# Kernel optimization log

Measured on AMD Instinct MI355X. Metric: run time of the kernel, lower is better.

## Reference

```python
import jax, jax.numpy as jnp
import numpy as np

HIDDEN = 1024
HEADS = 16
HEAD_DIM = HIDDEN // HEADS  # 64
ROPE_BASE = 10000.0
CLAMP = 10000.0


def _rope_cos_sin(seq_len, dtype=jnp.float32):
    inv_freq = 1.0 / (ROPE_BASE ** (jnp.arange(0, HEAD_DIM, 2, dtype=dtype) / HEAD_DIM))
    t = jnp.arange(seq_len, dtype=dtype)
    freqs = jnp.outer(t, inv_freq)  # [T, HEAD_DIM//2]
    return jnp.cos(freqs), jnp.sin(freqs)


def _apply_rope(x, cos, sin):
    # x: [B, H, T, HEAD_DIM]; cos/sin: [T, HEAD_DIM//2]
    x1, x2 = jnp.split(x, 2, axis=-1)
    cos = cos[None, None]
    sin = sin[None, None]
    return jnp.concatenate([x1 * cos - x2 * sin, x1 * sin + x2 * cos], axis=-1)


def setup_inputs() -> dict:
    key = jax.random.key(0)
    ks = jax.random.split(key, 5)
    B, T, D = 2, 2048, HIDDEN
    x = jax.random.normal(ks[0], (B, T, D), dtype=jnp.float32)
    # torch Linear weights are [out, in]; init std=0.02, zero bias
    Wq = jax.random.normal(ks[1], (D, D), dtype=jnp.float32) * 0.02
    Wk = jax.random.normal(ks[2], (D, D), dtype=jnp.float32) * 0.02
    Wv = jax.random.normal(ks[3], (D, D), dtype=jnp.float32) * 0.02
    Wo = jax.random.normal(ks[4], (D, D), dtype=jnp.float32) * 0.02
    bq = jnp.zeros((D,), jnp.float32)
    bk = jnp.zeros((D,), jnp.float32)
    bv = jnp.zeros((D,), jnp.float32)
    bo = jnp.zeros((D,), jnp.float32)
    # causal mask: True where attention is disallowed (strict upper triangle)
    causal_mask = jnp.triu(jnp.ones((T, T), dtype=bool), k=1)[None, None]
    return {"x": x, "causal_mask": causal_mask,
            "Wq": Wq, "bq": bq, "Wk": Wk, "bk": bk,
            "Wv": Wv, "bv": bv, "Wo": Wo, "bo": bo}


def reference(x, causal_mask, Wq, bq, Wk, bk, Wv, bv, Wo, bo):
    B, T, D = x.shape
    H, hd = HEADS, HEAD_DIM

    def proj(W, b):
        y = jnp.einsum('btd,ed->bte', x, W) + b
        return y.reshape(B, T, H, hd).transpose(0, 2, 1, 3)  # [B,H,T,hd]

    q = proj(Wq, bq)
    k = proj(Wk, bk)
    v = proj(Wv, bv)

    cos, sin = _rope_cos_sin(T, x.dtype)
    q = _apply_rope(q, cos, sin)
    k = _apply_rope(k, cos, sin)

    scores = jnp.einsum('bhqd,bhkd->bhqk', q, k) / jnp.sqrt(jnp.asarray(hd, x.dtype))
    # masked_fill(-inf) happens BEFORE clamp, so masked entries become -10000
    scores = jnp.where(causal_mask[:, :, :T, :T], -jnp.inf, scores)
    scores = jnp.clip(scores, -CLAMP, CLAMP)
    attn = jax.nn.softmax(scores, axis=-1)
    out = jnp.einsum('bhqk,bhkd->bhqd', attn, v)
    out = out.transpose(0, 2, 1, 3).reshape(B, T, D)
    return jnp.einsum('btd,ed->bte', out, Wo) + bo
```

## Files before the change

kernel.cpp:

```cpp
#include <hip/hip_runtime.h>
#include <hip/hip_bf16.h>
#include <math.h>

#define T_SEQ   2048
#define D_MOD   1024
#define N_HEADS 16
#define HEAD_DIM 64
#define B_BATCH 2
#define M_ROWS  (B_BATCH * T_SEQ)

typedef unsigned short u16;
typedef unsigned int u32;
typedef __attribute__((ext_vector_type(8))) short short8;
typedef __attribute__((ext_vector_type(4))) float floatx4;
typedef __attribute__((ext_vector_type(16))) float f32x16;
typedef __attribute__((ext_vector_type(4))) u32 u32x4;

__device__ inline floatx4 mfma16(short8 a, short8 b, floatx4 c) {
  return __builtin_amdgcn_mfma_f32_16x16x32_bf16(a, b, c, 0, 0, 0);
}
__device__ inline f32x16 mfma32(short8 a, short8 b, f32x16 c) {
  return __builtin_amdgcn_mfma_f32_32x32x16_bf16(a, b, c, 0, 0, 0);
}

__device__ inline u16 f2bf(float f) {
  __hip_bfloat16 h = __float2bfloat16(f);
  return __builtin_bit_cast(u16, h);
}
__device__ inline u32 pack2bf(float lo, float hi) {
  return (u32)f2bf(lo) | ((u32)f2bf(hi) << 16);
}

__device__ inline void gload16(const void* g, void* s) {
  __builtin_amdgcn_global_load_lds(
      (const __attribute__((address_space(1))) void*)g,
      (__attribute__((address_space(3))) void*)s, 16, 0, 0);
}

__global__ void cast_all_kernel(const float* __restrict__ x,
                                const float* __restrict__ Wq, const float* __restrict__ Wk,
                                const float* __restrict__ Wv, const float* __restrict__ Wo,
                                u16* __restrict__ Xb, u16* __restrict__ Wqb, u16* __restrict__ Wkb,
                                u16* __restrict__ Wvb, u16* __restrict__ Wob) {
  size_t i4 = ((size_t)blockIdx.x * 256 + threadIdx.x) * 4;
  size_t seg = i4 >> 20;
  const float* src; u16* dst; size_t off;
  if (seg < 4)       { src = x;  dst = Xb;  off = i4; }
  else if (seg == 4) { src = Wq; dst = Wqb; off = i4 - ((size_t)4 << 20); }
  else if (seg == 5) { src = Wk; dst = Wkb; off = i4 - ((size_t)5 << 20); }
  else if (seg == 6) { src = Wv; dst = Wvb; off = i4 - ((size_t)6 << 20); }
  else               { src = Wo; dst = Wob; off = i4 - ((size_t)7 << 20); }
  float4 v = *(const float4*)(src + off);
  ushort4 o;
  o.x = f2bf(v.x); o.y = f2bf(v.y); o.z = f2bf(v.z); o.w = f2bf(v.w);
  *(ushort4*)(dst + off) = o;
}

__global__ void rope_table_kernel(float* __restrict__ cosT, float* __restrict__ sinT) {
  int tid = blockIdx.x * blockDim.x + threadIdx.x;
  int t = tid >> 5, j = tid & 31;
  double inv = pow(10000.0, -((double)(2 * j) / 64.0));
  double a = (double)t * inv;
  cosT[tid] = (float)cos(a);
  sinT[tid] = (float)sin(a);
}

template<int OUT_BF16, int DO_ROPE>
__global__ __launch_bounds__(256) void gemm128_kernel(
    const u16* __restrict__ A,
    const u16* __restrict__ W0, const u16* __restrict__ W1, const u16* __restrict__ W2,
    const float* __restrict__ b0, const float* __restrict__ b1, const float* __restrict__ b2,
    void* __restrict__ C0, void* __restrict__ C1, void* __restrict__ C2,
    const float* __restrict__ cosT, const float* __restrict__ sinT) {
  const int z = blockIdx.z;
  const u16*  W    = (z == 0) ? W0 : (z == 1 ? W1 : W2);
  const float* bias = (z == 0) ? b0 : (z == 1 ? b1 : b2);
  void*       C    = (z == 0) ? C0 : (z == 1 ? C1 : C2);
  const int K = D_MOD, N = D_MOD;

  __shared__ __align__(16) char smem[34816];
  u16* lA0 = (u16*)smem;
  u16* lA1 = (u16*)(smem + 8192);
  u16* lB0 = (u16*)(smem + 16384);
  u16* lB1 = (u16*)(smem + 24576);

  const int tid = threadIdx.x;
  const int w = tid >> 6, l = tid & 63, g = l >> 4, ln = l & 15;
  const int wr = w >> 1, wc = w & 1;
  const int m0 = blockIdx.y * 128, n0 = blockIdx.x * 128;

  floatx4 acc[4][4];
#pragma unroll
  for (int mi = 0; mi < 4; ++mi)
#pragma unroll
    for (int ni = 0; ni < 4; ++ni) acc[mi][ni] = (floatx4){0.f, 0.f, 0.f, 0.f};

  auto stage = [&](u16* la, u16* lb, int kk) {
#pragma unroll
    for (int p = 0; p < 2; ++p) {
      int c = p * 256 + w * 64 + l;
      int r = c >> 2, cc = c & 3;
      gload16(A + (size_t)(m0 + r) * K + kk + cc * 8, la + (p * 256 + w * 64) * 8);
      gload16(W + (size_t)(n0 + r) * K + kk + cc * 8, lb + (p * 256 + w * 64) * 8);
    }
  };

  stage(lA0, lB0, 0);
  __syncthreads();
  for (int t = 0; t < K / 32; ++t) {
    u16* la = (t & 1) ? lA1 : lA0;
    u16* lb = (t & 1) ? lB1 : lB0;
    if (t + 1 < K / 32) stage((t & 1) ? lA0 : lA1, (t & 1) ? lB0 : lB1, (t + 1) * 32);
    short8 af[4], bf[4];
#pragma unroll
    for (int mi = 0; mi < 4; ++mi)
      af[mi] = *(const short8*)&la[(wr * 64 + mi * 16 + ln) * 32 + g * 8];
#pragma unroll
    for (int ni = 0; ni < 4; ++ni)
      bf[ni] = *(const short8*)&lb[(wc * 64 + ni * 16 + ln) * 32 + g * 8];
#pragma unroll
    for (int mi = 0; mi < 4; ++mi)
#pragma unroll
      for (int ni = 0; ni < 4; ++ni)
        acc[mi][ni] = mfma16(af[mi], bf[ni], acc[mi][ni]);
    __syncthreads();
  }

  float bv[4];
#pragma unroll
  for (int ni = 0; ni < 4; ++ni) bv[ni] = bias[n0 + wc * 64 + ni * 16 + ln];

  if (DO_ROPE && z == 2) {
    u16* pt = (u16*)smem;
#pragma unroll
    for (int mi = 0; mi < 4; ++mi)
#pragma unroll
      for (int ni = 0; ni < 4; ++ni)
#pragma unroll
        for (int r = 0; r < 4; ++r)
          pt[(wc * 64 + ni * 16 + ln) * 136 + wr * 64 + mi * 16 + g * 4 + r] =
              f2bf(acc[mi][ni][r] + bv[ni]);
    __syncthreads();
    u16* Vt = (u16*)C;
    const int b = m0 >> 11, tc0 = m0 & (T_SEQ - 1);
#pragma unroll
    for (int i = 0; i < 8; ++i) {
      const int c = tid + 256 * i;
      const int row = c >> 4, mc = c & 15;
      const int n = n0 + row;
      const int hh = n >> 6, d = n & 63;
      short8 val = *(const short8*)&pt[row * 136 + mc * 8];
      *(short8*)(Vt + ((size_t)(b * N_HEADS + hh) * 64 + d) * T_SEQ + tc0 + mc * 8) = val;
    }
    return;
  }

#pragma unroll
  for (int mi = 0; mi < 4; ++mi) {
#pragma unroll
    for (int r = 0; r < 4; ++r) {
      const int m = m0 + wr * 64 + mi * 16 + g * 4 + r;
      if (DO_ROPE && z < 2) {
        const int t = m & (T_SEQ - 1);
#pragma unroll
        for (int ni = 0; ni < 2; ++ni) {
          const int j = ni * 16 + ln;
          float cv = cosT[t * 32 + j], sv = sinT[t * 32 + j];
          float v1 = acc[mi][ni][r] + bv[ni];
          float v2 = acc[mi][ni + 2][r] + bv[ni + 2];
          ((u16*)C)[(size_t)m * N + n0 + wc * 64 + j]      = f2bf(v1 * cv - v2 * sv);
          ((u16*)C)[(size_t)m * N + n0 + wc * 64 + j + 32] = f2bf(v1 * sv + v2 * cv);
        }
      } else {
#pragma unroll
        for (int ni = 0; ni < 4; ++ni) {
          float v = acc[mi][ni][r] + bv[ni];
          size_t idx = (size_t)m * N + n0 + wc * 64 + ni * 16 + ln;
          if (OUT_BF16) ((u16*)C)[idx] = f2bf(v);
          else          ((float*)C)[idx] = v;
        }
      }
    }
  }
}

__global__ __launch_bounds__(256) void flash7_kernel(const u16* __restrict__ Q, const u16* __restrict__ Kb,
                                                     const u16* __restrict__ Vt, u16* __restrict__ O) {
  __shared__ float og[3][32][64];
  __shared__ float mlg[3][2][64];

  const int tid = threadIdx.x;
  const int w = tid >> 6, l = tid & 63;
  const int lq = l & 31, hi = l >> 5;

  const int orig = blockIdx.x;
  const int wg = (orig & 7) * 256 + (orig >> 3);
  const int bh = wg >> 6;
  const int qt = 63 - (wg & 63);
  const int q0 = qt * 32;
  const int b = bh >> 4, h = bh & 15;

  const u16* Qh = Q  + (size_t)b * T_SEQ * D_MOD + h * HEAD_DIM;
  const u16* Kh = Kb + (size_t)b * T_SEQ * D_MOD + h * HEAD_DIM;
  const u16* Vh = Vt + (size_t)bh * 64 * T_SEQ;

  short8 qf[4];
  {
    const u16* qp = Qh + (size_t)(q0 + lq) * D_MOD + 8 * hi;
#pragma unroll
    for (int j = 0; j < 4; ++j) qf[j] = *(const short8*)(qp + 16 * j);
  }

  f32x16 o0, o1;
#pragma unroll
  for (int r = 0; r < 16; ++r) { o0[r] = 0.f; o1[r] = 0.f; }
  float m_r = -INFINITY, l_r = 0.f;

  const int ntiles = (qt >> 1) + 1;
  for (int kt = w; kt < ntiles; kt += 4) {
    const int k0 = kt * 64;
    const bool last = (kt == ntiles - 1);

    short8 kf0[4], kf1[4], vf0[4], vf1[4];
    {
      const u16* kp0 = Kh + (size_t)(k0 + lq) * D_MOD + 8 * hi;
      const u16* kp1 = kp0 + 32 * D_MOD;
#pragma unroll
      for (int j = 0; j < 4; ++j) {
        kf0[j] = *(const short8*)(kp0 + 16 * j);
        kf1[j] = *(const short8*)(kp1 + 16 * j);
      }
      const u16* vp0 = Vh + (size_t)lq * T_SEQ + k0 + 8 * hi;
      const u16* vp1 = vp0 + 32 * T_SEQ;
#pragma unroll
      for (int js = 0; js < 4; ++js) {
        vf0[js] = *(const short8*)(vp0 + 16 * js);
        vf1[js] = *(const short8*)(vp1 + 16 * js);
      }
    }

    f32x16 s0, s1;
#pragma unroll
    for (int r = 0; r < 16; ++r) { s0[r] = 0.f; s1[r] = 0.f; }
    __builtin_amdgcn_s_setprio(1);
#pragma unroll
    for (int j = 0; j < 4; ++j) {
      s0 = mfma32(kf0[j], qf[j], s0);
      s1 = mfma32(kf1[j], qf[j], s1);
    }
    __builtin_amdgcn_s_setprio(0);

    float p[32];
#pragma unroll
    for (int r = 0; r < 16; ++r) { p[r] = s0[r] * 0.125f; p[16 + r] = s1[r] * 0.125f; }
    if (last) {
      const int qrow = q0 + lq;
#pragma unroll
      for (int r = 0; r < 16; ++r) {
        const int kv = k0 + (r & 3) + 8 * (r >> 2) + 4 * hi;
        if (kv > qrow) p[r] = -10000.0f;
        if (kv + 32 > qrow) p[16 + r] = -10000.0f;
      }
    }

    float mx = p[0];
#pragma unroll
    for (int i = 1; i < 32; ++i) mx = fmaxf(mx, p[i]);
    mx = fmaxf(mx, __shfl_xor(mx, 32));

    const float mnew = fmaxf(m_r, mx);
    const float alpha = __expf(m_r - mnew);
    l_r *= alpha;
#pragma unroll
    for (int r = 0; r < 16; ++r) { o0[r] *= alpha; o1[r] *= alpha; }
    m_r = mnew;
#pragma unroll
    for (int i = 0; i < 32; ++i) p[i] = __expf(p[i] - m_r);
    float sum = 0.f;
#pragma unroll
    for (int i = 0; i < 32; ++i) sum += p[i];
    sum += __shfl_xor(sum, 32);
    l_r += sum;

    u32x4 fw[4];
#pragma unroll
    for (int a = 0; a < 2; ++a) {
      u32 W[8];
#pragma unroll
      for (int j = 0; j < 8; ++j) W[j] = pack2bf(p[16 * a + 2 * j], p[16 * a + 2 * j + 1]);
      u32 A0 = __shfl_xor(hi ? W[0] : W[2], 32);
      u32 A1 = __shfl_xor(hi ? W[1] : W[3], 32);
      u32 B0 = __shfl_xor(hi ? W[4] : W[6], 32);
      u32 B1 = __shfl_xor(hi ? W[5] : W[7], 32);
      fw[2 * a]     = (u32x4){hi ? A0 : W[0], hi ? A1 : W[1], hi ? W[2] : A0, hi ? W[3] : A1};
      fw[2 * a + 1] = (u32x4){hi ? B0 : W[4], hi ? B1 : W[5], hi ? W[6] : B0, hi ? W[7] : B1};
    }

    __builtin_amdgcn_s_setprio(1);
#pragma unroll
    for (int js = 0; js < 4; ++js) {
      short8 pf = __builtin_bit_cast(short8, fw[js]);
      o0 = mfma32(vf0[js], pf, o0);
      o1 = mfma32(vf1[js], pf, o1);
    }
    __builtin_amdgcn_s_setprio(0);
  }

  if (w > 0) {
    mlg[w - 1][0][l] = m_r;
    mlg[w - 1][1][l] = l_r;
#pragma unroll
    for (int r = 0; r < 16; ++r) {
      og[w - 1][r][l]      = o0[r];
      og[w - 1][16 + r][l] = o1[r];
    }
  }
  __syncthreads();
  if (w != 0) return;

  float m = m_r;
#pragma unroll
  for (int pi = 0; pi < 3; ++pi) m = fmaxf(m, mlg[pi][0][l]);
  const float aS = __expf(m_r - m);
  float lsum = l_r * aS;
#pragma unroll
  for (int r = 0; r < 16; ++r) { o0[r] *= aS; o1[r] *= aS; }
#pragma unroll
  for (int pi = 0; pi < 3; ++pi) {
    const float ap = __expf(mlg[pi][0][l] - m);
    lsum += mlg[pi][1][l] * ap;
#pragma unroll
    for (int r = 0; r < 16; ++r) {
      o0[r] += og[pi][r][l] * ap;
      o1[r] += og[pi][16 + r][l] * ap;
    }
  }

  const float inv = 1.0f / lsum;
  u16* op = O + (size_t)b * T_SEQ * D_MOD + (size_t)(q0 + lq) * D_MOD + h * HEAD_DIM;
#pragma unroll
  for (int a = 0; a < 2; ++a) {
#pragma unroll
    for (int rq = 0; rq < 4; ++rq) {
      const int d0 = 32 * a + 8 * rq + 4 * hi;
      ushort4 st;
      st.x = f2bf(((a == 0) ? o0[4 * rq + 0] : o1[4 * rq + 0]) * inv);
      st.y = f2bf(((a == 0) ? o0[4 * rq + 1] : o1[4 * rq + 1]) * inv);
      st.z = f2bf(((a == 0) ? o0[4 * rq + 2] : o1[4 * rq + 2]) * inv);
      st.w = f2bf(((a == 0) ? o0[4 * rq + 3] : o1[4 * rq + 3]) * inv);
      *(ushort4*)(op + d0) = st;
    }
  }
}

extern "C" void kernel_launch(void* const* d_in, const int* in_sizes, int n_in,
                              void* d_out, int out_size, void* d_ws, size_t ws_size,
                              hipStream_t stream) {
  const float* x  = (const float*)d_in[0];
  const float* Wq = (const float*)d_in[2];
  const float* bq = (const float*)d_in[3];
  const float* Wk = (const float*)d_in[4];
  const float* bk = (const float*)d_in[5];
  const float* Wv = (const float*)d_in[6];
  const float* bv = (const float*)d_in[7];
  const float* Wo = (const float*)d_in[8];
  const float* bo = (const float*)d_in[9];
  float* out = (float*)d_out;

  char* ws = (char*)d_ws;
  const size_t MB = 1024 * 1024;
  u16* Xb   = (u16*)(ws + 0);
  u16* Ab   = (u16*)(ws + 0);
  u16* Wqb  = (u16*)(ws + 8 * MB);
  u16* Wkb  = (u16*)(ws + 10 * MB);
  u16* Wvb  = (u16*)(ws + 12 * MB);
  u16* Wob  = (u16*)(ws + 14 * MB);
  u16* Qb   = (u16*)(ws + 16 * MB);
  u16* Kb   = (u16*)(ws + 24 * MB);
  u16* Vt   = (u16*)(ws + 32 * MB);
  float* cosT = (float*)(ws + 48 * MB);
  float* sinT = (float*)(ws + 48 * MB + 256 * 1024);

  cast_all_kernel<<<8192, 256, 0, stream>>>(x, Wq, Wk, Wv, Wo, Xb, Wqb, Wkb, Wvb, Wob);
  rope_table_kernel<<<256, 256, 0, stream>>>(cosT, sinT);

  gemm128_kernel<1, 1><<<dim3(8, 32, 3), 256, 0, stream>>>(
      Xb, Wqb, Wkb, Wvb, bq, bk, bv, Qb, Kb, Vt, cosT, sinT);

  flash7_kernel<<<dim3(2048), 256, 0, stream>>>(Qb, Kb, Vt, Ab);

  gemm128_kernel<0, 0><<<dim3(8, 32, 1), 256, 0, stream>>>(
      Ab, Wob, Wob, Wob, bo, bo, bo, out, out, out, nullptr, nullptr);
}
```

Measured before the change: 238.3 us.

## Store Q/K/V in per-head 8-element-chunk slabs for coalesced attention loads

The QKV projection epilogue now writes Q, K and V into a per-(batch,head) slab layout where each 16-byte chunk of head dimensions is stored contiguously across time. The flash kernel loads its MFMA fragments from these slabs, so each wavefront reads contiguous 512-byte runs instead of 16-byte pieces strided by the full model width or sequence length. This is meant to cut memory transactions and cache-line waste in the attention kernel. The trade-off is that the RoPE epilogue stores become scattered 2-byte writes across far-apart slab planes, which may slow the projection GEMM.

```diff
diff --git a/kernel.cpp b/kernel.cpp
--- a/kernel.cpp
+++ b/kernel.cpp
@@ -8,6 +8,7 @@
 #define HEAD_DIM 64
 #define B_BATCH 2
 #define M_ROWS  (B_BATCH * T_SEQ)
+#define HSLAB   131072
 
 typedef unsigned short u16;
 typedef unsigned int u32;
@@ -141,16 +142,17 @@
           pt[(wc * 64 + ni * 16 + ln) * 136 + wr * 64 + mi * 16 + g * 4 + r] =
               f2bf(acc[mi][ni][r] + bv[ni]);
     __syncthreads();
-    u16* Vt = (u16*)C;
+    u16* Vz = (u16*)C;
     const int b = m0 >> 11, tc0 = m0 & (T_SEQ - 1);
 #pragma unroll
     for (int i = 0; i < 8; ++i) {
       const int c = tid + 256 * i;
-      const int row = c >> 4, mc = c & 15;
-      const int n = n0 + row;
-      const int hh = n >> 6, d = n & 63;
-      short8 val = *(const short8*)&pt[row * 136 + mc * 8];
-      *(short8*)(Vt + ((size_t)(b * N_HEADS + hh) * 64 + d) * T_SEQ + tc0 + mc * 8) = val;
+      const int drow = c & 63;
+      const int hloc = (c >> 6) & 1;
+      const int mc = c >> 7;
+      const int bh = b * N_HEADS + ((n0 + hloc * 64) >> 6);
+      short8 val = *(const short8*)&pt[(hloc * 64 + drow) * 136 + mc * 8];
+      *(short8*)(Vz + (size_t)bh * HSLAB + (size_t)((tc0 >> 3) + mc) * 512 + drow * 8) = val;
     }
     return;
   }
@@ -162,14 +164,16 @@
       const int m = m0 + wr * 64 + mi * 16 + g * 4 + r;
       if (DO_ROPE && z < 2) {
         const int t = m & (T_SEQ - 1);
+        const int bh = (m >> 11) * N_HEADS + ((n0 + wc * 64) >> 6);
+        u16* base = (u16*)C + (size_t)bh * HSLAB + (size_t)t * 8;
 #pragma unroll
         for (int ni = 0; ni < 2; ++ni) {
           const int j = ni * 16 + ln;
           float cv = cosT[t * 32 + j], sv = sinT[t * 32 + j];
           float v1 = acc[mi][ni][r] + bv[ni];
           float v2 = acc[mi][ni + 2][r] + bv[ni + 2];
-          ((u16*)C)[(size_t)m * N + n0 + wc * 64 + j]      = f2bf(v1 * cv - v2 * sv);
-          ((u16*)C)[(size_t)m * N + n0 + wc * 64 + j + 32] = f2bf(v1 * sv + v2 * cv);
+          base[(j >> 3) * 16384 + (j & 7)]       = f2bf(v1 * cv - v2 * sv);
+          base[((j >> 3) + 4) * 16384 + (j & 7)] = f2bf(v1 * sv + v2 * cv);
         }
       } else {
 #pragma unroll
@@ -184,8 +188,8 @@
   }
 }
 
-__global__ __launch_bounds__(256) void flash7_kernel(const u16* __restrict__ Q, const u16* __restrict__ Kb,
-                                                     const u16* __restrict__ Vt, u16* __restrict__ O) {
+__global__ __launch_bounds__(256) void flash8_kernel(const u16* __restrict__ Q, const u16* __restrict__ Kb,
+                                                     const u16* __restrict__ Vb, u16* __restrict__ O) {
   __shared__ float og[3][32][64];
   __shared__ float mlg[3][2][64];
 
@@ -200,16 +204,14 @@
   const int q0 = qt * 32;
   const int b = bh >> 4, h = bh & 15;
 
-  const u16* Qh = Q  + (size_t)b * T_SEQ * D_MOD + h * HEAD_DIM;
-  const u16* Kh = Kb + (size_t)b * T_SEQ * D_MOD + h * HEAD_DIM;
-  const u16* Vh = Vt + (size_t)bh * 64 * T_SEQ;
+  const u16* Qz = Q  + (size_t)bh * HSLAB;
+  const u16* Kz = Kb + (size_t)bh * HSLAB;
+  const u16* Vz = Vb + (size_t)bh * HSLAB;
 
   short8 qf[4];
-  {
-    const u16* qp = Qh + (size_t)(q0 + lq) * D_MOD + 8 * hi;
-#pragma unroll
-    for (int j = 0; j < 4; ++j) qf[j] = *(const short8*)(qp + 16 * j);
-  }
+#pragma unroll
+  for (int j = 0; j < 4; ++j)
+    qf[j] = *(const short8*)(Qz + (size_t)(2 * j + hi) * 16384 + (q0 + lq) * 8);
 
   f32x16 o0, o1;
 #pragma unroll
@@ -223,19 +225,17 @@
 
     short8 kf0[4], kf1[4], vf0[4], vf1[4];
     {
-      const u16* kp0 = Kh + (size_t)(k0 + lq) * D_MOD + 8 * hi;
-      const u16* kp1 = kp0 + 32 * D_MOD;
+      const u16* kp = Kz + (size_t)hi * 16384 + (k0 + lq) * 8;
 #pragma unroll
       for (int j = 0; j < 4; ++j) {
-        kf0[j] = *(const short8*)(kp0 + 16 * j);
-        kf1[j] = *(const short8*)(kp1 + 16 * j);
+        kf0[j] = *(const short8*)(kp + (size_t)(2 * j) * 16384);
+        kf1[j] = *(const short8*)(kp + (size_t)(2 * j) * 16384 + 256);
       }
-      const u16* vp0 = Vh + (size_t)lq * T_SEQ + k0 + 8 * hi;
-      const u16* vp1 = vp0 + 32 * T_SEQ;
+      const u16* vp = Vz + (size_t)((k0 >> 3) + hi) * 512 + lq * 8;
 #pragma unroll
       for (int js = 0; js < 4; ++js) {
-        vf0[js] = *(const short8*)(vp0 + 16 * js);
-        vf1[js] = *(const short8*)(vp1 + 16 * js);
+        vf0[js] = *(const short8*)(vp + (size_t)(2 * js) * 512);
+        vf1[js] = *(const short8*)(vp + (size_t)(2 * js) * 512 + 256);
       }
     }
 
@@ -377,7 +377,7 @@
   u16* Wob  = (u16*)(ws + 14 * MB);
   u16* Qb   = (u16*)(ws + 16 * MB);
   u16* Kb   = (u16*)(ws + 24 * MB);
-  u16* Vt   = (u16*)(ws + 32 * MB);
+  u16* Vb   = (u16*)(ws + 32 * MB);
   float* cosT = (float*)(ws + 48 * MB);
   float* sinT = (float*)(ws + 48 * MB + 256 * 1024);
 
@@ -385,9 +385,9 @@
   rope_table_kernel<<<256, 256, 0, stream>>>(cosT, sinT);
 
   gemm128_kernel<1, 1><<<dim3(8, 32, 3), 256, 0, stream>>>(
-      Xb, Wqb, Wkb, Wvb, bq, bk, bv, Qb, Kb, Vt, cosT, sinT);
-
-  flash7_kernel<<<dim3(2048), 256, 0, stream>>>(Qb, Kb, Vt, Ab);
+      Xb, Wqb, Wkb, Wvb, bq, bk, bv, Qb, Kb, Vb, cosT, sinT);
+
+  flash8_kernel<<<dim3(2048), 256, 0, stream>>>(Qb, Kb, Vb, Ab);
 
   gemm128_kernel<0, 0><<<dim3(8, 32, 1), 256, 0, stream>>>(
       Ab, Wob, Wob, Wob, bo, bo, bo, out, out, out, nullptr, nullptr);
```

Result: faster. 205.0 us (-14.0%).
